# Performance work log

Measured on AMD Instinct MI355X. Metric: run time of the kernel, lower is better.

## Reference

```python
import jax, jax.numpy as jnp
import numpy as np

B, C, H, W = 4, 8, 64, 64
C8 = C // 8  # = 1, required for the residual broadcast in PAM


def _conv1x1(x, w, b):
    # x: [B,C,H,W], w: [O,C], b: [O] -> [B,O,H,W]
    return jnp.einsum('bchw,oc->bohw', x, w) + b[None, :, None, None]


def setup_inputs() -> dict:
    key = jax.random.key(0)
    ks = jax.random.split(key, 13)
    s_c = 1.0 / np.sqrt(C)
    inp = {'x': jax.random.normal(ks[0], (B, C, H, W), jnp.float32)}
    # CAM: three 1x1 convs C->C
    inp['cam_wq'] = jax.random.normal(ks[1], (C, C), jnp.float32) * s_c
    inp['cam_bq'] = jnp.zeros((C,), jnp.float32)
    inp['cam_wk'] = jax.random.normal(ks[2], (C, C), jnp.float32) * s_c
    inp['cam_bk'] = jnp.zeros((C,), jnp.float32)
    inp['cam_wv'] = jax.random.normal(ks[3], (C, C), jnp.float32) * s_c
    inp['cam_bv'] = jnp.zeros((C,), jnp.float32)
    # PAM: three 1x1 convs C->C//8
    inp['pam_wq'] = jax.random.normal(ks[4], (C8, C), jnp.float32) * s_c
    inp['pam_bq'] = jnp.zeros((C8,), jnp.float32)
    inp['pam_wk'] = jax.random.normal(ks[5], (C8, C), jnp.float32) * s_c
    inp['pam_bk'] = jnp.zeros((C8,), jnp.float32)
    inp['pam_wv'] = jax.random.normal(ks[6], (C8, C), jnp.float32) * s_c
    inp['pam_bv'] = jnp.zeros((C8,), jnp.float32)
    return inp


def reference(x, cam_wq, cam_bq, cam_wk, cam_bk, cam_wv, cam_bv,
              pam_wq, pam_bq, pam_wk, pam_bk, pam_wv, pam_bv):
    b, c, h, w = x.shape
    hw = h * w

    # ---- Channel Attention Module (C x C attention) ----
    q = _conv1x1(x, cam_wq, cam_bq).reshape(b, c, hw)            # [B,C,HW]
    k = _conv1x1(x, cam_wk, cam_bk).reshape(b, c, hw)            # [B,C,HW]
    v = _conv1x1(x, cam_wv, cam_bv).reshape(b, c, hw)            # [B,C,HW]
    attn_c = jax.nn.softmax(jnp.einsum('bcn,bdn->bcd', q, k), axis=-1)  # [B,C,C]
    out_cam = jnp.einsum('bcd,bdn->bcn', attn_c, v).reshape(b, c, h, w) + x

    # ---- Pixel Attention Module (HW x HW attention, C//8 channels) ----
    pq = _conv1x1(x, pam_wq, pam_bq).reshape(b, -1, hw)          # [B,C8,HW]
    pk = _conv1x1(x, pam_wk, pam_bk).reshape(b, -1, hw)          # [B,C8,HW]
    pv = _conv1x1(x, pam_wv, pam_bv).reshape(b, -1, hw)          # [B,C8,HW]
    attn_p = jax.nn.softmax(jnp.einsum('bcn,bcm->bnm', pq, pk), axis=-1)  # [B,HW,HW]
    # out = v @ attn^T  -> [B,C8,HW]; residual broadcasts C8=1 against C
    out_p = jnp.einsum('bcm,bnm->bcn', pv, attn_p).reshape(b, c // 8, h, w)
    out_pam = out_p + x                                          # broadcast [B,1,H,W]+[B,C,H,W]

    return out_pam + out_cam
```

## Files before the change

kernel.cpp:

```cpp
#include <hip/hip_runtime.h>

#define CC 8
#define HW 4096
#define L2E 1.4426950408889634f

#define PART_OFF 0
#define PQ_OFF   4096
#define PK2_OFF  20480
#define PV_OFF   36864

typedef __attribute__((ext_vector_type(4))) float f32x4;

__global__ __launch_bounds__(256) void k1_stats(
    const float* __restrict__ x,
    const float* __restrict__ pwq, const float* __restrict__ pbq,
    const float* __restrict__ pwk, const float* __restrict__ pbk,
    const float* __restrict__ pwv, const float* __restrict__ pbv,
    float* __restrict__ ws)
{
  const int b = blockIdx.x >> 4, chunk = blockIdx.x & 15;
  const int tid = threadIdx.x;
  const int n = chunk * 256 + tid;
  const float* xb = x + b * CC * HW;

  float wqv[CC], wkv[CC], wvv[CC];
  #pragma unroll
  for (int c = 0; c < CC; ++c) { wqv[c] = pwq[c]; wkv[c] = pwk[c]; wvv[c] = pwv[c]; }

  float xv[CC];
  #pragma unroll
  for (int c = 0; c < CC; ++c) xv[c] = xb[c * HW + n];

  float pq = pbq[0], pk = pbk[0], pv = pbv[0];
  #pragma unroll
  for (int c = 0; c < CC; ++c) {
    pq = fmaf(wqv[c], xv[c], pq);
    pk = fmaf(wkv[c], xv[c], pk);
    pv = fmaf(wvv[c], xv[c], pv);
  }
  ws[PQ_OFF  + b * HW + n] = pq;
  ws[PK2_OFF + b * HW + n] = pk * L2E;
  ws[PV_OFF  + b * HW + n] = pv;

  float acc[44];
  {
    int k = 0;
    #pragma unroll
    for (int c = 0; c < CC; ++c) {
      #pragma unroll
      for (int d = c; d < CC; ++d) { acc[k] = xv[c] * xv[d]; ++k; }
    }
    #pragma unroll
    for (int c = 0; c < CC; ++c) acc[36 + c] = xv[c];
  }

  #pragma unroll
  for (int i = 0; i < 44; ++i) {
    float v = acc[i];
    #pragma unroll
    for (int off = 32; off > 0; off >>= 1) v += __shfl_xor(v, off, 64);
    acc[i] = v;
  }

  __shared__ float part[4][44];
  const int wv_ = tid >> 6, ln = tid & 63;
  if (ln == 0) {
    #pragma unroll
    for (int i = 0; i < 44; ++i) part[wv_][i] = acc[i];
  }
  __syncthreads();
  if (tid < 44) {
    const float t = part[0][tid] + part[1][tid] + part[2][tid] + part[3][tid];
    ws[PART_OFF + (b * 16 + chunk) * 44 + tid] = t;
  }
}

__global__ __launch_bounds__(1024) void k3_main(
    const float* __restrict__ x,
    const float* __restrict__ cwq, const float* __restrict__ cbq,
    const float* __restrict__ cwk, const float* __restrict__ cbk,
    const float* __restrict__ cwv, const float* __restrict__ cbv,
    const float* __restrict__ ws, float* __restrict__ out)
{
  const int b = blockIdx.x >> 6, tile = blockIdx.x & 63;
  const int n0 = tile * 64;
  const int t = threadIdx.x, ln = t & 63;
  const int seg = __builtin_amdgcn_readfirstlane(t >> 6);

  __shared__ float redd[16][64], redn[16][64];
  __shared__ float sums[44], Gl[64], Ll[64], Al[64], Mp[64], cvs[8], outp[64];

  const float a = ws[PQ_OFF + b * HW + n0 + ln];

  const float* pkp = ws + PK2_OFF + b * HW + seg * 256;
  const float* pvp = ws + PV_OFF  + b * HW + seg * 256;

  float d0 = 0, d1 = 0, d2 = 0, d3 = 0;
  float m0 = 0, m1 = 0, m2 = 0, m3 = 0;

  for (int ch = 0; ch < 16; ++ch) {
    f32x4 k0, k1, k2, k3, v0, v1, v2, v3;
    asm volatile(
      "s_load_dwordx4 %0, %8, 0x0\n\t"
      "s_load_dwordx4 %1, %8, 0x10\n\t"
      "s_load_dwordx4 %2, %8, 0x20\n\t"
      "s_load_dwordx4 %3, %8, 0x30\n\t"
      "s_load_dwordx4 %4, %9, 0x0\n\t"
      "s_load_dwordx4 %5, %9, 0x10\n\t"
      "s_load_dwordx4 %6, %9, 0x20\n\t"
      "s_load_dwordx4 %7, %9, 0x30\n\t"
      "s_waitcnt lgkmcnt(0)"
      : "=&s"(k0), "=&s"(k1), "=&s"(k2), "=&s"(k3),
        "=&s"(v0), "=&s"(v1), "=&s"(v2), "=&s"(v3)
      : "s"(pkp), "s"(pvp));
    pkp += 16; pvp += 16;

#define GRP(kg, vg, dd, nn) {                               \
    float e0 = __builtin_amdgcn_exp2f(a * kg[0]);           \
    float e1 = __builtin_amdgcn_exp2f(a * kg[1]);           \
    float e2 = __builtin_amdgcn_exp2f(a * kg[2]);           \
    float e3 = __builtin_amdgcn_exp2f(a * kg[3]);           \
    dd += ((e0 + e1) + (e2 + e3));                          \
    nn = fmaf(e0, vg[0], nn); nn = fmaf(e1, vg[1], nn);     \
    nn = fmaf(e2, vg[2], nn); nn = fmaf(e3, vg[3], nn); }

    GRP(k0, v0, d0, m0)
    GRP(k1, v1, d1, m1)
    GRP(k2, v2, d2, m2)
    GRP(k3, v3, d3, m3)
#undef GRP
  }

  redd[seg][ln] = (d0 + d1) + (d2 + d3);
  redn[seg][ln] = (m0 + m1) + (m2 + m3);
  __syncthreads();

  if (t < 64) {
    float D = 0.f, N = 0.f;
    #pragma unroll
    for (int s = 0; s < 16; ++s) { D += redd[s][t]; N += redn[s][t]; }
    outp[t] = N / D;
  }
  if (t < 44) {
    float s = 0.f;
    for (int ch = 0; ch < 16; ++ch) s += ws[PART_OFF + (b * 16 + ch) * 44 + t];
    sums[t] = s;
  }
  __syncthreads();

  const int c = ln >> 3, d = ln & 7;
  if (t < 64) {
    const int lo = min(c, d), hi = max(c, d);
    Gl[t] = sums[lo * 8 + hi - lo * (lo + 1) / 2];
  }
  __syncthreads();

  float Lv = 0.f;
  if (t < 64) {
    float qs = 0.f, ks = 0.f;
    #pragma unroll
    for (int e = 0; e < 8; ++e) {
      qs = fmaf(cwq[c * 8 + e], sums[36 + e], qs);
      ks = fmaf(cwk[d * 8 + e], sums[36 + e], ks);
    }
    float A = 0.f;
    #pragma unroll
    for (int e = 0; e < 8; ++e) {
      float inner = 0.f;
      #pragma unroll
      for (int f = 0; f < 8; ++f) inner = fmaf(Gl[e * 8 + f], cwk[d * 8 + f], inner);
      A = fmaf(cwq[c * 8 + e], inner, A);
    }
    Lv = A + qs * cbk[d] + cbq[c] * ks + 4096.f * cbq[c] * cbk[d];
    Ll[t] = Lv;
  }
  __syncthreads();

  if (t < 64) {
    float mx = -INFINITY;
    #pragma unroll
    for (int f = 0; f < 8; ++f) mx = fmaxf(mx, Ll[c * 8 + f]);
    float ssum = 0.f;
    #pragma unroll
    for (int f = 0; f < 8; ++f) ssum += __expf(Ll[c * 8 + f] - mx);
    Al[t] = __expf(Lv - mx) / ssum;
  }
  __syncthreads();

  if (t < 64) {
    float M = 0.f;
    #pragma unroll
    for (int f = 0; f < 8; ++f) M = fmaf(Al[c * 8 + f], cwv[f * 8 + d], M);
    if (d == c) M += 2.f;
    Mp[t] = M;
    if (d == 0) {
      float cvv = 0.f;
      #pragma unroll
      for (int f = 0; f < 8; ++f) cvv = fmaf(Al[c * 8 + f], cbv[f], cvv);
      cvs[c] = cvv;
    }
  }
  __syncthreads();

  if (t < 512) {
    const int w = seg;
    float xv[8];
    #pragma unroll
    for (int dd = 0; dd < 8; ++dd) xv[dd] = x[(b * 8 + dd) * HW + n0 + ln];
    float o = cvs[w] + outp[ln];
    #pragma unroll
    for (int dd = 0; dd < 8; ++dd) o = fmaf(Mp[w * 8 + dd], xv[dd], o);
    out[(b * 8 + w) * HW + n0 + ln] = o;
  }
}

extern "C" void kernel_launch(void* const* d_in, const int* in_sizes, int n_in,
                              void* d_out, int out_size, void* d_ws, size_t ws_size,
                              hipStream_t stream) {
  const float* x   = (const float*)d_in[0];
  const float* cwq = (const float*)d_in[1];
  const float* cbq = (const float*)d_in[2];
  const float* cwk = (const float*)d_in[3];
  const float* cbk = (const float*)d_in[4];
  const float* cwv = (const float*)d_in[5];
  const float* cbv = (const float*)d_in[6];
  const float* pwq = (const float*)d_in[7];
  const float* pbq = (const float*)d_in[8];
  const float* pwk = (const float*)d_in[9];
  const float* pbk = (const float*)d_in[10];
  const float* pwv = (const float*)d_in[11];
  const float* pbv = (const float*)d_in[12];
  float* ws  = (float*)d_ws;
  float* out = (float*)d_out;

  hipLaunchKernelGGL(k1_stats, dim3(64), dim3(256), 0, stream,
                     x, pwq, pbq, pwk, pbk, pwv, pbv, ws);
  hipLaunchKernelGGL(k3_main, dim3(256), dim3(1024), 0, stream,
                     x, cwq, cbq, cwk, cbk, cwv, cbv, ws, out);
}
```

Measured before the change: 23.82 us.

## Fuse stats and attention kernels, recompute PAM projections per block into LDS

Merges the two kernels into one. Each block recomputes the per-pixel PAM key and value projections for its whole batch image into an interleaved LDS buffer, and recomputes the Gram and channel sums redundantly with four waves. This removes a kernel launch, the workspace round trip and the scalar-load streaming of K and V. The cost is redundant work: every one of the 64 tiles per batch reads the full x image and recomputes the projections and the Gram matrix, and the block now uses 32KB of LDS.

```diff
diff --git a/kernel.cpp b/kernel.cpp
--- a/kernel.cpp
+++ b/kernel.cpp
@@ -4,135 +4,118 @@
 #define HW 4096
 #define L2E 1.4426950408889634f
 
-#define PART_OFF 0
-#define PQ_OFF   4096
-#define PK2_OFF  20480
-#define PV_OFF   36864
-
 typedef __attribute__((ext_vector_type(4))) float f32x4;
 
-__global__ __launch_bounds__(256) void k1_stats(
-    const float* __restrict__ x,
-    const float* __restrict__ pwq, const float* __restrict__ pbq,
-    const float* __restrict__ pwk, const float* __restrict__ pbk,
-    const float* __restrict__ pwv, const float* __restrict__ pbv,
-    float* __restrict__ ws)
-{
-  const int b = blockIdx.x >> 4, chunk = blockIdx.x & 15;
-  const int tid = threadIdx.x;
-  const int n = chunk * 256 + tid;
-  const float* xb = x + b * CC * HW;
-
-  float wqv[CC], wkv[CC], wvv[CC];
-  #pragma unroll
-  for (int c = 0; c < CC; ++c) { wqv[c] = pwq[c]; wkv[c] = pwk[c]; wvv[c] = pwv[c]; }
-
-  float xv[CC];
-  #pragma unroll
-  for (int c = 0; c < CC; ++c) xv[c] = xb[c * HW + n];
-
-  float pq = pbq[0], pk = pbk[0], pv = pbv[0];
-  #pragma unroll
-  for (int c = 0; c < CC; ++c) {
-    pq = fmaf(wqv[c], xv[c], pq);
-    pk = fmaf(wkv[c], xv[c], pk);
-    pv = fmaf(wvv[c], xv[c], pv);
-  }
-  ws[PQ_OFF  + b * HW + n] = pq;
-  ws[PK2_OFF + b * HW + n] = pk * L2E;
-  ws[PV_OFF  + b * HW + n] = pv;
-
-  float acc[44];
-  {
-    int k = 0;
-    #pragma unroll
-    for (int c = 0; c < CC; ++c) {
-      #pragma unroll
-      for (int d = c; d < CC; ++d) { acc[k] = xv[c] * xv[d]; ++k; }
-    }
-    #pragma unroll
-    for (int c = 0; c < CC; ++c) acc[36 + c] = xv[c];
-  }
-
-  #pragma unroll
-  for (int i = 0; i < 44; ++i) {
-    float v = acc[i];
-    #pragma unroll
-    for (int off = 32; off > 0; off >>= 1) v += __shfl_xor(v, off, 64);
-    acc[i] = v;
-  }
-
-  __shared__ float part[4][44];
-  const int wv_ = tid >> 6, ln = tid & 63;
-  if (ln == 0) {
-    #pragma unroll
-    for (int i = 0; i < 44; ++i) part[wv_][i] = acc[i];
-  }
-  __syncthreads();
-  if (tid < 44) {
-    const float t = part[0][tid] + part[1][tid] + part[2][tid] + part[3][tid];
-    ws[PART_OFF + (b * 16 + chunk) * 44 + tid] = t;
-  }
-}
-
-__global__ __launch_bounds__(1024) void k3_main(
+__global__ __launch_bounds__(1024, 4) void fused_attn(
     const float* __restrict__ x,
     const float* __restrict__ cwq, const float* __restrict__ cbq,
     const float* __restrict__ cwk, const float* __restrict__ cbk,
     const float* __restrict__ cwv, const float* __restrict__ cbv,
-    const float* __restrict__ ws, float* __restrict__ out)
+    const float* __restrict__ pwq, const float* __restrict__ pbq,
+    const float* __restrict__ pwk, const float* __restrict__ pbk,
+    const float* __restrict__ pwv, const float* __restrict__ pbv,
+    float* __restrict__ out)
 {
   const int b = blockIdx.x >> 6, tile = blockIdx.x & 63;
   const int n0 = tile * 64;
   const int t = threadIdx.x, ln = t & 63;
-  const int seg = __builtin_amdgcn_readfirstlane(t >> 6);
-
+  const int wid = __builtin_amdgcn_readfirstlane(t >> 6);
+
+  __shared__ __align__(16) float kv[HW * 2];
   __shared__ float redd[16][64], redn[16][64];
+  __shared__ float gpart[4][44];
   __shared__ float sums[44], Gl[64], Ll[64], Al[64], Mp[64], cvs[8], outp[64];
 
-  const float a = ws[PQ_OFF + b * HW + n0 + ln];
-
-  const float* pkp = ws + PK2_OFF + b * HW + seg * 256;
-  const float* pvp = ws + PV_OFF  + b * HW + seg * 256;
-
-  float d0 = 0, d1 = 0, d2 = 0, d3 = 0;
-  float m0 = 0, m1 = 0, m2 = 0, m3 = 0;
-
-  for (int ch = 0; ch < 16; ++ch) {
-    f32x4 k0, k1, k2, k3, v0, v1, v2, v3;
-    asm volatile(
-      "s_load_dwordx4 %0, %8, 0x0\n\t"
-      "s_load_dwordx4 %1, %8, 0x10\n\t"
-      "s_load_dwordx4 %2, %8, 0x20\n\t"
-      "s_load_dwordx4 %3, %8, 0x30\n\t"
-      "s_load_dwordx4 %4, %9, 0x0\n\t"
-      "s_load_dwordx4 %5, %9, 0x10\n\t"
-      "s_load_dwordx4 %6, %9, 0x20\n\t"
-      "s_load_dwordx4 %7, %9, 0x30\n\t"
-      "s_waitcnt lgkmcnt(0)"
-      : "=&s"(k0), "=&s"(k1), "=&s"(k2), "=&s"(k3),
-        "=&s"(v0), "=&s"(v1), "=&s"(v2), "=&s"(v3)
-      : "s"(pkp), "s"(pvp));
-    pkp += 16; pvp += 16;
-
-#define GRP(kg, vg, dd, nn) {                               \
-    float e0 = __builtin_amdgcn_exp2f(a * kg[0]);           \
-    float e1 = __builtin_amdgcn_exp2f(a * kg[1]);           \
-    float e2 = __builtin_amdgcn_exp2f(a * kg[2]);           \
-    float e3 = __builtin_amdgcn_exp2f(a * kg[3]);           \
-    dd += ((e0 + e1) + (e2 + e3));                          \
-    nn = fmaf(e0, vg[0], nn); nn = fmaf(e1, vg[1], nn);     \
-    nn = fmaf(e2, vg[2], nn); nn = fmaf(e3, vg[3], nn); }
-
-    GRP(k0, v0, d0, m0)
-    GRP(k1, v1, d1, m1)
-    GRP(k2, v2, d2, m2)
-    GRP(k3, v3, d3, m3)
-#undef GRP
-  }
-
-  redd[seg][ln] = (d0 + d1) + (d2 + d3);
-  redn[seg][ln] = (m0 + m1) + (m2 + m3);
+  const float* xb = x + b * CC * HW;
+
+  {
+    const int m4 = t * 4;
+    f32x4 xc[CC];
+    #pragma unroll
+    for (int c = 0; c < CC; ++c)
+      xc[c] = *(const f32x4*)(xb + c * HW + m4);
+    f32x4 kk, vv;
+    #pragma unroll
+    for (int j = 0; j < 4; ++j) {
+      float k = pbk[0], v = pbv[0];
+      #pragma unroll
+      for (int c = 0; c < CC; ++c) {
+        k = fmaf(pwk[c], xc[c][j], k);
+        v = fmaf(pwv[c], xc[c][j], v);
+      }
+      kk[j] = k * L2E; vv[j] = v;
+    }
+    f32x4* kv4 = (f32x4*)kv;
+    f32x4 w0, w1;
+    w0[0] = kk[0]; w0[1] = vv[0]; w0[2] = kk[1]; w0[3] = vv[1];
+    w1[0] = kk[2]; w1[1] = vv[2]; w1[2] = kk[3]; w1[3] = vv[3];
+    kv4[2 * t] = w0; kv4[2 * t + 1] = w1;
+  }
+
+  float xn[CC];
+  #pragma unroll
+  for (int c = 0; c < CC; ++c) xn[c] = xb[c * HW + n0 + ln];
+  float a = pbq[0];
+  #pragma unroll
+  for (int c = 0; c < CC; ++c) a = fmaf(pwq[c], xn[c], a);
+
+  if (wid < 4) {
+    float acc[44];
+    #pragma unroll
+    for (int i = 0; i < 44; ++i) acc[i] = 0.f;
+    const int p0 = t * 16;
+    #pragma unroll
+    for (int blk = 0; blk < 4; ++blk) {
+      f32x4 xq[CC];
+      #pragma unroll
+      for (int c = 0; c < CC; ++c)
+        xq[c] = *(const f32x4*)(xb + c * HW + p0 + blk * 4);
+      #pragma unroll
+      for (int j = 0; j < 4; ++j) {
+        int k = 0;
+        #pragma unroll
+        for (int c = 0; c < CC; ++c) {
+          #pragma unroll
+          for (int d = c; d < CC; ++d) { acc[k] = fmaf(xq[c][j], xq[d][j], acc[k]); ++k; }
+        }
+        #pragma unroll
+        for (int c = 0; c < CC; ++c) acc[36 + c] += xq[c][j];
+      }
+    }
+    #pragma unroll
+    for (int i = 0; i < 44; ++i) {
+      float v = acc[i];
+      #pragma unroll
+      for (int off = 32; off > 0; off >>= 1) v += __shfl_xor(v, off, 64);
+      acc[i] = v;
+    }
+    if (ln == 0) {
+      #pragma unroll
+      for (int i = 0; i < 44; ++i) gpart[wid][i] = acc[i];
+    }
+  }
+  __syncthreads();
+
+  {
+    const f32x4* kvw = ((const f32x4*)kv) + (wid << 7);
+    float dA = 0, dB = 0, dC = 0, dD = 0;
+    float nA = 0, nB = 0, nC = 0, nD = 0;
+    #pragma unroll 2
+    for (int i = 0; i < 128; i += 4) {
+      const f32x4 p0 = kvw[i], p1 = kvw[i + 1], p2 = kvw[i + 2], p3 = kvw[i + 3];
+      float e;
+      e = __builtin_amdgcn_exp2f(a * p0[0]); dA += e; nA = fmaf(e, p0[1], nA);
+      e = __builtin_amdgcn_exp2f(a * p0[2]); dA += e; nA = fmaf(e, p0[3], nA);
+      e = __builtin_amdgcn_exp2f(a * p1[0]); dB += e; nB = fmaf(e, p1[1], nB);
+      e = __builtin_amdgcn_exp2f(a * p1[2]); dB += e; nB = fmaf(e, p1[3], nB);
+      e = __builtin_amdgcn_exp2f(a * p2[0]); dC += e; nC = fmaf(e, p2[1], nC);
+      e = __builtin_amdgcn_exp2f(a * p2[2]); dC += e; nC = fmaf(e, p2[3], nC);
+      e = __builtin_amdgcn_exp2f(a * p3[0]); dD += e; nD = fmaf(e, p3[1], nD);
+      e = __builtin_amdgcn_exp2f(a * p3[2]); dD += e; nD = fmaf(e, p3[3], nD);
+    }
+    redd[wid][ln] = (dA + dB) + (dC + dD);
+    redn[wid][ln] = (nA + nB) + (nC + nD);
+  }
   __syncthreads();
 
   if (t < 64) {
@@ -141,11 +124,8 @@
     for (int s = 0; s < 16; ++s) { D += redd[s][t]; N += redn[s][t]; }
     outp[t] = N / D;
   }
-  if (t < 44) {
-    float s = 0.f;
-    for (int ch = 0; ch < 16; ++ch) s += ws[PART_OFF + (b * 16 + ch) * 44 + t];
-    sums[t] = s;
-  }
+  if (t < 44)
+    sums[t] = gpart[0][t] + gpart[1][t] + gpart[2][t] + gpart[3][t];
   __syncthreads();
 
   const int c = ln >> 3, d = ln & 7;
@@ -203,13 +183,10 @@
   __syncthreads();
 
   if (t < 512) {
-    const int w = seg;
-    float xv[8];
-    #pragma unroll
-    for (int dd = 0; dd < 8; ++dd) xv[dd] = x[(b * 8 + dd) * HW + n0 + ln];
+    const int w = wid;
     float o = cvs[w] + outp[ln];
     #pragma unroll
-    for (int dd = 0; dd < 8; ++dd) o = fmaf(Mp[w * 8 + dd], xv[dd], o);
+    for (int dd = 0; dd < 8; ++dd) o = fmaf(Mp[w * 8 + dd], xn[dd], o);
     out[(b * 8 + w) * HW + n0 + ln] = o;
   }
 }
@@ -230,11 +207,9 @@
   const float* pbk = (const float*)d_in[10];
   const float* pwv = (const float*)d_in[11];
   const float* pbv = (const float*)d_in[12];
-  float* ws  = (float*)d_ws;
   float* out = (float*)d_out;
 
-  hipLaunchKernelGGL(k1_stats, dim3(64), dim3(256), 0, stream,
-                     x, pwq, pbq, pwk, pbk, pwv, pbv, ws);
-  hipLaunchKernelGGL(k3_main, dim3(256), dim3(1024), 0, stream,
-                     x, cwq, cbq, cwk, cbk, cwv, cbv, ws, out);
+  hipLaunchKernelGGL(fused_attn, dim3(256), dim3(1024), 0, stream,
+                     x, cwq, cbq, cwk, cbk, cwv, cbv,
+                     pwq, pbq, pwk, pbk, pwv, pbv, out);
 }
```

Result: slower. 44.28 us (+85.9%).
